# Performance work log

Measured on AMD Instinct MI355X. Metric: run time of the kernel, lower is better.

The kernel has to match this reference:

```python
import jax, jax.numpy as jnp
import numpy as np

B, T, C, NH = 4, 2048, 1024, 16
HD = C // NH  # head dim = 64


def setup_inputs() -> dict:
    key = jax.random.key(0)
    ks = jax.random.split(key, 5)
    s = 0.02
    return {
        "x": jax.random.normal(ks[0], (B, T, C), dtype=jnp.float32),
        "W_attn": jax.random.normal(ks[1], (C, 3 * C), dtype=jnp.float32) * s,
        "b_attn": jnp.zeros((3 * C,), dtype=jnp.float32),
        "W_proj": jax.random.normal(ks[2], (C, C), dtype=jnp.float32) * s,
        "b_proj": jnp.zeros((C,), dtype=jnp.float32),
    }


def reference(x, W_attn, b_attn, W_proj, b_proj):
    Bv, Tv, Cv = x.shape
    qkv = x @ W_attn + b_attn  # [B,T,3C]
    q, k, v = jnp.split(qkv, 3, axis=2)
    # [B,T,C] -> [B,NH,T,HD]
    def heads(t):
        return t.reshape(Bv, Tv, NH, HD).transpose(0, 2, 1, 3)
    q, k, v = heads(q), heads(k), heads(v)
    scores = jnp.einsum("bhqd,bhkd->bhqk", q, k) / jnp.sqrt(jnp.float32(HD))
    causal = jnp.tril(jnp.ones((Tv, Tv), dtype=bool))
    scores = jnp.where(causal[None, None, :, :], scores, jnp.float32(-jnp.inf))
    probs = jax.nn.softmax(scores, axis=-1)
    # dropout rate is 0.0 -> identity
    y = jnp.einsum("bhqk,bhkd->bhqd", probs, v)
    y = y.transpose(0, 2, 1, 3).reshape(Bv, Tv, Cv)
    return y @ W_proj + b_proj
```

## Files before the change

### kernel.cpp

```cpp
#include <hip/hip_runtime.h>
#include <hip/hip_bf16.h>

#define Bsz 4
#define Tseq 2048
#define Cdim 1024
#define NH 16
#define HD 64
#define Mrows (Bsz*Tseq)
#define N3C (3*Cdim)

typedef __attribute__((ext_vector_type(8))) short short8;
typedef __attribute__((ext_vector_type(4))) short short4v;
typedef __attribute__((ext_vector_type(4))) float float4v;

__device__ __forceinline__ unsigned short f2b(float f) {
    union { float f; unsigned u; } x; x.f = f;
    unsigned u = x.u;
    u += 0x7fff + ((u >> 16) & 1);
    return (unsigned short)(u >> 16);
}

__device__ __forceinline__ unsigned pk2bf(float a, float b) {
#if __has_builtin(__builtin_amdgcn_cvt_pk_bf16_f32)
    auto w = __builtin_amdgcn_cvt_pk_bf16_f32(a, b);
    unsigned u; __builtin_memcpy(&u, &w, 4);
    return u;
#else
    return (unsigned)f2b(a) | ((unsigned)f2b(b) << 16);
#endif
}

#define GLDS(gp, lp) __builtin_amdgcn_global_load_lds(                         \
    (const __attribute__((address_space(1))) unsigned*)(gp),                   \
    (__attribute__((address_space(3))) unsigned*)(lp), 16, 0, 0)

__global__ __launch_bounds__(256) void cast_kernel(const float* __restrict__ in,
                                                   unsigned short* __restrict__ out, int n) {
    int i = (blockIdx.x * 256 + threadIdx.x) * 4;
    if (i < n) {
        float4 v = *reinterpret_cast<const float4*>(in + i);
        ushort4 o;
        o.x = f2b(v.x); o.y = f2b(v.y); o.z = f2b(v.z); o.w = f2b(v.w);
        *reinterpret_cast<ushort4*>(out + i) = o;
    }
}

__global__ __launch_bounds__(256) void transpose_cast(const float* __restrict__ in,
                                                      unsigned short* __restrict__ out,
                                                      int K, int N) {
    __shared__ float tile[32][33];
    int n0 = blockIdx.x * 32, k0 = blockIdx.y * 32;
    int tx = threadIdx.x & 31, ty = threadIdx.x >> 5;
    #pragma unroll
    for (int i = 0; i < 32; i += 8)
        tile[ty + i][tx] = in[(k0 + ty + i) * N + n0 + tx];
    __syncthreads();
    #pragma unroll
    for (int i = 0; i < 32; i += 8)
        out[(size_t)(n0 + ty + i) * K + k0 + tx] = f2b(tile[tx][ty + i]);
}


template<bool QKV>
__global__ __launch_bounds__(512, 2) void gemm256(const unsigned short* __restrict__ A,
                                                  const unsigned short* __restrict__ Bt,
                                                  const float* __restrict__ bias,
                                                  unsigned short* __restrict__ qb,
                                                  unsigned short* __restrict__ kb,
                                                  unsigned short* __restrict__ vb,
                                                  float* __restrict__ out) {
    __shared__ unsigned short As[3][256 * 64];
    __shared__ unsigned short Bs[3][128 * 64];

    int tid = threadIdx.x;
    int lane = tid & 63, wave = tid >> 6;
    int wm = wave >> 2, wn = wave & 3;
    int l15 = lane & 15, quad = lane >> 4;
    int sx = l15 & 7;

    int f = blockIdx.x;
    int xcd = f & 7, slot = f >> 3;
    int rowblk = xcd * 4 + (slot & 3);
    int colblk = slot >> 2;
    int row0 = rowblk * 256;
    int col0 = colblk * 128;

    int srow = lane >> 3;
    int gsw = ((lane & 7) ^ srow) * 8;
    const unsigned short* Ag = A + (size_t)(row0 + wave * 32 + srow) * Cdim + gsw;
    const unsigned short* Bg = Bt + (size_t)(col0 + wave * 16 + srow) * Cdim + gsw;

    float4v acc[8][2] = {};

    #define STAGE256(kk, sb) do {                                              \
        unsigned short* Al = &As[sb][wave * 32 * 64];                          \
        unsigned short* Bl = &Bs[sb][wave * 16 * 64];                          \
        GLDS(Ag + (kk), Al);                                                   \
        GLDS(Ag + (kk) + (size_t)8  * Cdim, Al + 8 * 64);                      \
        GLDS(Ag + (kk) + (size_t)16 * Cdim, Al + 16 * 64);                     \
        GLDS(Ag + (kk) + (size_t)24 * Cdim, Al + 24 * 64);                     \
        GLDS(Bg + (kk), Bl);                                                   \
        GLDS(Bg + (kk) + (size_t)8  * Cdim, Bl + 8 * 64);                      \
    } while (0)

    STAGE256(0, 0);
    STAGE256(64, 1);
    asm volatile("s_waitcnt vmcnt(6)" ::: "memory");
    __builtin_amdgcn_s_barrier();

    int bc = 0, bp = 2;
    #pragma unroll 1
    for (int t = 0; t < 16; ++t) {
        int kpre = ((t + 2) & 15) * 64;
        STAGE256(kpre, bp);

        const unsigned short* Asb = &As[bc][0];
        const unsigned short* Bsb = &Bs[bc][0];
        #pragma unroll
        for (int kg = 0; kg < 2; kg++) {
            int gcol = ((kg * 4 + quad) ^ sx) * 8;
            short8 af[8], bf[2];
            #pragma unroll
            for (int mi = 0; mi < 8; mi++)
                af[mi] = *(const short8*)&Asb[(wm * 128 + mi * 16 + l15) * 64 + gcol];
            #pragma unroll
            for (int ni = 0; ni < 2; ni++)
                bf[ni] = *(const short8*)&Bsb[(wn * 32 + ni * 16 + l15) * 64 + gcol];
            __builtin_amdgcn_s_setprio(1);
            #pragma unroll
            for (int mi = 0; mi < 8; mi++)
                #pragma unroll
                for (int ni = 0; ni < 2; ni++)
                    acc[mi][ni] = __builtin_amdgcn_mfma_f32_16x16x32_bf16(af[mi], bf[ni], acc[mi][ni], 0, 0, 0);
            __builtin_amdgcn_s_setprio(0);
        }

        asm volatile("s_waitcnt vmcnt(6)" ::: "memory");
        __builtin_amdgcn_s_barrier();
        bc = (bc == 2) ? 0 : bc + 1;
        bp = (bp == 2) ? 0 : bp + 1;
    }
    #undef STAGE256

    #pragma unroll
    for (int mi = 0; mi < 8; mi++) {
        #pragma unroll
        for (int ni = 0; ni < 2; ni++) {
            int colb = col0 + wn * 32 + ni * 16 + l15;
            int rowb = row0 + wm * 128 + mi * 16 + quad * 4;
            if (QKV) {
                int p = colb >> 10;
                int h = (colb & 1023) >> 6;
                int d = colb & 63;
                int b = rowb >> 11;
                int t = rowb & 2047;
                if (p == 2) {
                    ushort4 pk;
                    pk.x = f2b(acc[mi][ni][0] + bias[colb]);
                    pk.y = f2b(acc[mi][ni][1] + bias[colb]);
                    pk.z = f2b(acc[mi][ni][2] + bias[colb]);
                    pk.w = f2b(acc[mi][ni][3] + bias[colb]);
                    *(ushort4*)&vb[((size_t)(b * NH + h) * HD + d) * Tseq + t] = pk;
                } else {
                    unsigned short* dst = (p == 0) ? qb : kb;
                    #pragma unroll
                    for (int r = 0; r < 4; r++)
                        dst[((size_t)(b * NH + h) * Tseq + (t + r)) * HD + d] =
                            f2b(acc[mi][ni][r] + bias[colb]);
                }
            } else {
                #pragma unroll
                for (int r = 0; r < 4; r++)
                    out[(size_t)(rowb + r) * Cdim + colb] = acc[mi][ni][r] + bias[colb];
            }
        }
    }
}


__global__ __launch_bounds__(256, 4) void attn_kernel(const unsigned short* __restrict__ qb,
                                                      const unsigned short* __restrict__ kb,
                                                      const unsigned short* __restrict__ vt,
                                                      unsigned short* __restrict__ yb) {
    __shared__ unsigned short Ks[2][64 * 64];
    __shared__ unsigned short Vs[2][64 * 64];

    int tid = threadIdx.x;
    int lane = tid & 63, wave = tid >> 6;
    int l15 = lane & 15, quad = lane >> 4;
    int bh = blockIdx.x;
    int qt = 15 - blockIdx.y;

    const unsigned short* Qh = qb + (size_t)bh * Tseq * HD;
    const unsigned short* Kh = kb + (size_t)bh * Tseq * HD;
    const unsigned short* Vh = vt + (size_t)bh * HD * Tseq;
    int b = bh >> 4, h = bh & 15;
    const float cexp = 0.18033688011112042f;

    int q0 = qt * 128;
    int rb0 = q0 + wave * 32;

    short8 qf[2][2];
    #pragma unroll
    for (int mi = 0; mi < 2; mi++)
        #pragma unroll
        for (int g = 0; g < 2; g++)
            qf[mi][g] = *(const short8*)(Qh + (size_t)(rb0 + mi * 16 + l15) * HD + g * 32 + quad * 8);

    int srow = lane >> 3;
    int scol = ((lane & 7) ^ srow) * 8;
    const unsigned short* Kg0 = Kh + (size_t)(wave * 16 + srow) * HD + scol;
    const unsigned short* Vg0 = Vh + (size_t)(wave * 16 + srow) * Tseq + scol;
    unsigned short* Kl0 = &Ks[0][wave * 1024];
    unsigned short* Vl0 = &Vs[0][wave * 1024];
    unsigned short* Kl1 = &Ks[1][wave * 1024];
    unsigned short* Vl1 = &Vs[1][wave * 1024];

    int sx = l15 & 7;
    int kx0 = (quad ^ sx) * 8;
    int kx1 = ((4 + quad) ^ sx) * 8;
    int qh_ = quad >> 1, ql_ = quad & 1;

    float4v ov[2][4] = {};
    float m[2]  = {-1e30f, -1e30f};
    float lp[2] = {0.f, 0.f};

    int nw = (q0 >> 6) + 2;

    GLDS(Kg0, Kl0);                GLDS(Kg0 + 8 * HD, Kl0 + 512);
    GLDS(Vg0, Vl0);                GLDS(Vg0 + 8 * Tseq, Vl0 + 512);
    __syncthreads();

    #pragma unroll 1
    for (int it = 0; it < nw; ++it) {
        int j0 = it << 6;

        if (it + 1 < nw) {
            int jn = j0 + 64;
            unsigned short* Kl = (it & 1) ? Kl0 : Kl1;
            unsigned short* Vl = (it & 1) ? Vl0 : Vl1;
            GLDS(Kg0 + (size_t)jn * HD, Kl);
            GLDS(Kg0 + (size_t)(jn + 8) * HD, Kl + 512);
            GLDS(Vg0 + jn, Vl);
            GLDS(Vg0 + 8 * Tseq + jn, Vl + 512);
        }

        if (j0 <= rb0 + 31) {
            const unsigned short* Kl = &Ks[it & 1][0];
            const unsigned short* Vl = &Vs[it & 1][0];

            float4v st[2][4];
            #pragma unroll
            for (int mi = 0; mi < 2; mi++)
                #pragma unroll
                for (int kg = 0; kg < 4; kg++)
                    st[mi][kg] = (float4v){0.f, 0.f, 0.f, 0.f};
            #pragma unroll
            for (int kg = 0; kg < 4; kg++) {
                int krow = kg * 1024 + l15 * 64;
                short8 kf0 = *(const short8*)&Kl[krow + kx0];
                short8 kf1 = *(const short8*)&Kl[krow + kx1];
                st[0][kg] = __builtin_amdgcn_mfma_f32_16x16x32_bf16(kf0, qf[0][0], st[0][kg], 0, 0, 0);
                st[0][kg] = __builtin_amdgcn_mfma_f32_16x16x32_bf16(kf1, qf[0][1], st[0][kg], 0, 0, 0);
                st[1][kg] = __builtin_amdgcn_mfma_f32_16x16x32_bf16(kf0, qf[1][0], st[1][kg], 0, 0, 0);
                st[1][kg] = __builtin_amdgcn_mfma_f32_16x16x32_bf16(kf1, qf[1][1], st[1][kg], 0, 0, 0);
            }

            if (j0 + 63 > rb0) {
                #pragma unroll
                for (int mi = 0; mi < 2; mi++) {
                    int qrow = rb0 + mi * 16 + l15;
                    #pragma unroll
                    for (int kg = 0; kg < 4; kg++) {
                        int keyb = j0 + kg * 16 + quad * 4;
                        #pragma unroll
                        for (int r = 0; r < 4; r++)
                            if (keyb + r > qrow) st[mi][kg][r] = -1e30f;
                    }
                }
            }

            short4v pf[2][4];
            #pragma unroll
            for (int mi = 0; mi < 2; mi++) {
                float mx = st[mi][0][0];
                #pragma unroll
                for (int kg = 0; kg < 4; kg++)
                    #pragma unroll
                    for (int r = 0; r < 4; r++)
                        mx = fmaxf(mx, st[mi][kg][r]);
                mx = fmaxf(mx, __shfl_xor(mx, 16));
                mx = fmaxf(mx, __shfl_xor(mx, 32));
                if (__any(mx > m[mi] + 16.0f)) {
                    float mn = fmaxf(m[mi], mx);
                    float alv = __builtin_amdgcn_exp2f((m[mi] - mn) * cexp);
                    m[mi] = mn;
                    lp[mi] *= alv;
                    float ar_[4];
                    #pragma unroll
                    for (int r = 0; r < 4; r++)
                        ar_[r] = __shfl(alv, quad * 4 + r);
                    #pragma unroll
                    for (int dg = 0; dg < 4; dg++)
                        #pragma unroll
                        for (int r = 0; r < 4; r++)
                            ov[mi][dg][r] *= ar_[r];
                }
                float mc = -m[mi] * cexp;
                float sum = 0.f;
                #pragma unroll
                for (int kg = 0; kg < 4; kg++) {
                    float p0 = __builtin_amdgcn_exp2f(__builtin_fmaf(st[mi][kg][0], cexp, mc));
                    float p1 = __builtin_amdgcn_exp2f(__builtin_fmaf(st[mi][kg][1], cexp, mc));
                    float p2 = __builtin_amdgcn_exp2f(__builtin_fmaf(st[mi][kg][2], cexp, mc));
                    float p3 = __builtin_amdgcn_exp2f(__builtin_fmaf(st[mi][kg][3], cexp, mc));
                    sum += (p0 + p1) + (p2 + p3);
                    union { unsigned u[2]; short4v s; } pk_;
                    pk_.u[0] = pk2bf(p0, p1);
                    pk_.u[1] = pk2bf(p2, p3);
                    pf[mi][kg] = pk_.s;
                }
                lp[mi] += sum;
            }

            #pragma unroll
            for (int kg = 0; kg < 4; kg++) {
                int vx = (((kg * 2 + qh_) ^ sx) << 3) + ql_ * 4;
                #pragma unroll
                for (int dg = 0; dg < 4; dg++) {
                    short4v vf = *(const short4v*)&Vl[dg * 1024 + l15 * 64 + vx];
                    ov[0][dg] = __builtin_amdgcn_mfma_f32_16x16x16bf16_1k(pf[0][kg], vf, ov[0][dg], 0, 0, 0);
                    ov[1][dg] = __builtin_amdgcn_mfma_f32_16x16x16bf16_1k(pf[1][kg], vf, ov[1][dg], 0, 0, 0);
                }
            }
        }

        __syncthreads();
    }

    #pragma unroll
    for (int mi = 0; mi < 2; mi++) {
        float lf = lp[mi];
        lf += __shfl_xor(lf, 16);
        lf += __shfl_xor(lf, 32);
        float rinv[4];
        #pragma unroll
        for (int r = 0; r < 4; r++)
            rinv[r] = 1.0f / __shfl(lf, quad * 4 + r);
        #pragma unroll
        for (int dg = 0; dg < 4; dg++)
            #pragma unroll
            for (int r = 0; r < 4; r++) {
                int t = rb0 + mi * 16 + quad * 4 + r;
                yb[((size_t)b * Tseq + t) * Cdim + h * HD + dg * 16 + l15] =
                    f2b(ov[mi][dg][r] * rinv[r]);
            }
    }
}

extern "C" void kernel_launch(void* const* d_in, const int* in_sizes, int n_in,
                              void* d_out, int out_size, void* d_ws, size_t ws_size,
                              hipStream_t stream) {
    const float* x  = (const float*)d_in[0];
    const float* Wa = (const float*)d_in[1];
    const float* ba = (const float*)d_in[2];
    const float* Wp = (const float*)d_in[3];
    const float* bp = (const float*)d_in[4];
    float* out = (float*)d_out;

    unsigned short* ws = (unsigned short*)d_ws;
    unsigned short* xb  = ws;
    unsigned short* Wat = xb  + (size_t)Mrows * Cdim;
    unsigned short* Wpt = Wat + (size_t)N3C * Cdim;
    unsigned short* qb  = Wpt + (size_t)Cdim * Cdim;
    unsigned short* kb  = qb  + (size_t)Bsz * NH * Tseq * HD;
    unsigned short* vb  = kb  + (size_t)Bsz * NH * Tseq * HD;
    unsigned short* yb  = vb  + (size_t)Bsz * NH * Tseq * HD;

    int nx = Mrows * Cdim;
    cast_kernel<<<nx / 4 / 256, 256, 0, stream>>>(x, xb, nx);
    transpose_cast<<<dim3(N3C / 32, Cdim / 32), 256, 0, stream>>>(Wa, Wat, Cdim, N3C);
    transpose_cast<<<dim3(Cdim / 32, Cdim / 32), 256, 0, stream>>>(Wp, Wpt, Cdim, Cdim);

    gemm256<true><<<768, 512, 0, stream>>>(xb, Wat, ba, qb, kb, vb, nullptr);

    attn_kernel<<<dim3(Bsz * NH, 16), 256, 0, stream>>>(qb, kb, vb, yb);

    gemm256<false><<<256, 512, 0, stream>>>(yb, Wpt, bp, nullptr, nullptr, nullptr, out);
}
```

Before: 265.9 us.

## Add 256x256-tile QKV GEMM with eight-phase ping-pong LDS pipeline

```diff
diff --git a/kernel.cpp b/kernel.cpp
--- a/kernel.cpp
+++ b/kernel.cpp
@@ -62,6 +62,184 @@
 
 
 template<bool QKV>
+__global__ __launch_bounds__(512, 2) void gemm8p(const unsigned short* __restrict__ A,
+                                                 const unsigned short* __restrict__ Bt,
+                                                 const float* __restrict__ bias,
+                                                 unsigned short* __restrict__ qb,
+                                                 unsigned short* __restrict__ kb,
+                                                 unsigned short* __restrict__ vb,
+                                                 float* __restrict__ out) {
+    __shared__ unsigned short As[2][256 * 64];
+    __shared__ unsigned short Bs[2][256 * 64];
+
+    int tid = threadIdx.x;
+    int lane = tid & 63, wave = tid >> 6;
+    int wm = wave >> 2, wn = wave & 3;
+    int l15 = lane & 15, quad = lane >> 4;
+    int sx = l15 & 7;
+
+    int f = blockIdx.x;
+    int xcd = f & 7, slot = f >> 3;
+    int rowblk = xcd * 4 + (slot & 3);
+    int colblk = slot >> 2;
+    int row0 = rowblk * 256;
+    int col0 = colblk * 256;
+
+    int srow = lane >> 3;
+    int gsw = ((lane & 7) ^ srow) * 8;
+    const unsigned short* Ag = A + (size_t)(row0 + srow) * Cdim + gsw;
+    const unsigned short* Bg = Bt + (size_t)(col0 + srow) * Cdim + gsw;
+
+    #define STG_A(h, kk, nb) do {                                               \
+        unsigned short* L = &As[nb][((h) * 128 + wave * 8) * 64];               \
+        GLDS(Ag + (size_t)((h) * 128 + wave * 8) * Cdim + (kk), L);             \
+        GLDS(Ag + (size_t)((h) * 128 + 64 + wave * 8) * Cdim + (kk), L + 64 * 64); \
+    } while (0)
+    #define STG_B(h, kk, nb) do {                                               \
+        unsigned short* L = &Bs[nb][((h) * 128 + wave * 8) * 64];               \
+        GLDS(Bg + (size_t)((h) * 128 + wave * 8) * Cdim + (kk), L);             \
+        GLDS(Bg + (size_t)((h) * 128 + 64 + wave * 8) * Cdim + (kk), L + 64 * 64); \
+    } while (0)
+
+    float4v acc[8][4] = {};
+    short8 af0[8], af1[8];
+
+    STG_A(0, 0, 0); STG_A(1, 0, 0); STG_B(0, 0, 0); STG_B(1, 0, 0);
+    asm volatile("s_waitcnt vmcnt(0)" ::: "memory");
+    __builtin_amdgcn_s_barrier();
+
+    int gc0 = (quad ^ sx) * 8;
+    int gc1 = ((4 + quad) ^ sx) * 8;
+
+    #pragma unroll 1
+    for (int t = 0; t < 16; ++t) {
+        int b = t & 1, nb = b ^ 1;
+        int kn = ((t + 1) & 15) * 64;
+        const unsigned short* Asb = &As[b][0];
+        const unsigned short* Bsb = &Bs[b][0];
+
+        {
+            short8 bf[2];
+            #pragma unroll
+            for (int mi = 0; mi < 8; mi++)
+                af0[mi] = *(const short8*)&Asb[(wm * 128 + mi * 16 + l15) * 64 + gc0];
+            #pragma unroll
+            for (int ni = 0; ni < 2; ni++)
+                bf[ni] = *(const short8*)&Bsb[(wn * 64 + ni * 16 + l15) * 64 + gc0];
+            STG_A(0, kn, nb);
+            __builtin_amdgcn_s_barrier();
+            asm volatile("s_waitcnt lgkmcnt(0)" ::: "memory");
+            __builtin_amdgcn_sched_barrier(0);
+            __builtin_amdgcn_s_setprio(1);
+            #pragma unroll
+            for (int mi = 0; mi < 8; mi++)
+                #pragma unroll
+                for (int ni = 0; ni < 2; ni++)
+                    acc[mi][ni] = __builtin_amdgcn_mfma_f32_16x16x32_bf16(af0[mi], bf[ni], acc[mi][ni], 0, 0, 0);
+            __builtin_amdgcn_s_setprio(0);
+            __builtin_amdgcn_s_barrier();
+        }
+        {
+            short8 bf[2];
+            #pragma unroll
+            for (int mi = 0; mi < 8; mi++)
+                af1[mi] = *(const short8*)&Asb[(wm * 128 + mi * 16 + l15) * 64 + gc1];
+            #pragma unroll
+            for (int ni = 0; ni < 2; ni++)
+                bf[ni] = *(const short8*)&Bsb[(wn * 64 + ni * 16 + l15) * 64 + gc1];
+            STG_A(1, kn, nb);
+            asm volatile("s_waitcnt vmcnt(4)" ::: "memory");
+            __builtin_amdgcn_s_barrier();
+            asm volatile("s_waitcnt lgkmcnt(0)" ::: "memory");
+            __builtin_amdgcn_sched_barrier(0);
+            __builtin_amdgcn_s_setprio(1);
+            #pragma unroll
+            for (int mi = 0; mi < 8; mi++)
+                #pragma unroll
+                for (int ni = 0; ni < 2; ni++)
+                    acc[mi][ni] = __builtin_amdgcn_mfma_f32_16x16x32_bf16(af1[mi], bf[ni], acc[mi][ni], 0, 0, 0);
+            __builtin_amdgcn_s_setprio(0);
+            __builtin_amdgcn_s_barrier();
+        }
+        {
+            short8 bf[2];
+            #pragma unroll
+            for (int ni = 0; ni < 2; ni++)
+                bf[ni] = *(const short8*)&Bsb[(wn * 64 + 32 + ni * 16 + l15) * 64 + gc1];
+            STG_B(0, kn, nb);
+            __builtin_amdgcn_s_barrier();
+            asm volatile("s_waitcnt lgkmcnt(0)" ::: "memory");
+            __builtin_amdgcn_sched_barrier(0);
+            __builtin_amdgcn_s_setprio(1);
+            #pragma unroll
+            for (int mi = 0; mi < 8; mi++)
+                #pragma unroll
+                for (int ni = 0; ni < 2; ni++)
+                    acc[mi][2 + ni] = __builtin_amdgcn_mfma_f32_16x16x32_bf16(af1[mi], bf[ni], acc[mi][2 + ni], 0, 0, 0);
+            __builtin_amdgcn_s_setprio(0);
+            __builtin_amdgcn_s_barrier();
+        }
+        {
+            short8 bf[2];
+            #pragma unroll
+            for (int ni = 0; ni < 2; ni++)
+                bf[ni] = *(const short8*)&Bsb[(wn * 64 + 32 + ni * 16 + l15) * 64 + gc0];
+            STG_B(1, kn, nb);
+            asm volatile("s_waitcnt vmcnt(2)" ::: "memory");
+            __builtin_amdgcn_s_barrier();
+            asm volatile("s_waitcnt lgkmcnt(0)" ::: "memory");
+            __builtin_amdgcn_sched_barrier(0);
+            __builtin_amdgcn_s_setprio(1);
+            #pragma unroll
+            for (int mi = 0; mi < 8; mi++)
+                #pragma unroll
+                for (int ni = 0; ni < 2; ni++)
+                    acc[mi][2 + ni] = __builtin_amdgcn_mfma_f32_16x16x32_bf16(af0[mi], bf[ni], acc[mi][2 + ni], 0, 0, 0);
+            __builtin_amdgcn_s_setprio(0);
+            __builtin_amdgcn_s_barrier();
+        }
+    }
+    asm volatile("s_waitcnt vmcnt(0)" ::: "memory");
+    #undef STG_A
+    #undef STG_B
+
+    #pragma unroll
+    for (int mi = 0; mi < 8; mi++) {
+        #pragma unroll
+        for (int nj = 0; nj < 4; nj++) {
+            int colb = col0 + wn * 64 + nj * 16 + l15;
+            int rowb = row0 + wm * 128 + mi * 16 + quad * 4;
+            if (QKV) {
+                int p = colb >> 10;
+                int h = (colb & 1023) >> 6;
+                int d = colb & 63;
+                int b = rowb >> 11;
+                int t = rowb & 2047;
+                if (p == 2) {
+                    ushort4 pk;
+                    pk.x = f2b(acc[mi][nj][0] + bias[colb]);
+                    pk.y = f2b(acc[mi][nj][1] + bias[colb]);
+                    pk.z = f2b(acc[mi][nj][2] + bias[colb]);
+                    pk.w = f2b(acc[mi][nj][3] + bias[colb]);
+                    *(ushort4*)&vb[((size_t)(b * NH + h) * HD + d) * Tseq + t] = pk;
+                } else {
+                    unsigned short* dst = (p == 0) ? qb : kb;
+                    #pragma unroll
+                    for (int r = 0; r < 4; r++)
+                        dst[((size_t)(b * NH + h) * Tseq + (t + r)) * HD + d] =
+                            f2b(acc[mi][nj][r] + bias[colb]);
+                }
+            } else {
+                #pragma unroll
+                for (int r = 0; r < 4; r++)
+                    out[(size_t)(rowb + r) * Cdim + colb] = acc[mi][nj][r] + bias[colb];
+            }
+        }
+    }
+}
+
+
+template<bool QKV>
 __global__ __launch_bounds__(512, 2) void gemm256(const unsigned short* __restrict__ A,
                                                   const unsigned short* __restrict__ Bt,
                                                   const float* __restrict__ bias,
@@ -140,6 +318,7 @@
         bc = (bc == 2) ? 0 : bc + 1;
         bp = (bp == 2) ? 0 : bp + 1;
     }
+    asm volatile("s_waitcnt vmcnt(0)" ::: "memory");
     #undef STAGE256
 
     #pragma unroll
@@ -382,7 +561,7 @@
     transpose_cast<<<dim3(N3C / 32, Cdim / 32), 256, 0, stream>>>(Wa, Wat, Cdim, N3C);
     transpose_cast<<<dim3(Cdim / 32, Cdim / 32), 256, 0, stream>>>(Wp, Wpt, Cdim, Cdim);
 
-    gemm256<true><<<768, 512, 0, stream>>>(xb, Wat, ba, qb, kb, vb, nullptr);
+    gemm8p<true><<<384, 512, 0, stream>>>(xb, Wat, ba, qb, kb, vb, nullptr);
 
     attn_kernel<<<dim3(Bsz * NH, 16), 256, 0, stream>>>(qb, kb, vb, yb);
 
```

New measurement: 256.5 us. 1.04x faster.

## Restructure GEMM into four-phase ping-pong schedule with square 64x64 wave tiles

Applied to the files above, without the earlier changes.

```diff
diff --git a/kernel.cpp b/kernel.cpp
--- a/kernel.cpp
+++ b/kernel.cpp
@@ -62,19 +62,19 @@
 
 
 template<bool QKV>
-__global__ __launch_bounds__(512, 2) void gemm256(const unsigned short* __restrict__ A,
-                                                  const unsigned short* __restrict__ Bt,
-                                                  const float* __restrict__ bias,
-                                                  unsigned short* __restrict__ qb,
-                                                  unsigned short* __restrict__ kb,
-                                                  unsigned short* __restrict__ vb,
-                                                  float* __restrict__ out) {
+__global__ __launch_bounds__(512, 2) void gemm4p(const unsigned short* __restrict__ A,
+                                                 const unsigned short* __restrict__ Bt,
+                                                 const float* __restrict__ bias,
+                                                 unsigned short* __restrict__ qb,
+                                                 unsigned short* __restrict__ kb,
+                                                 unsigned short* __restrict__ vb,
+                                                 float* __restrict__ out) {
     __shared__ unsigned short As[3][256 * 64];
     __shared__ unsigned short Bs[3][128 * 64];
 
     int tid = threadIdx.x;
     int lane = tid & 63, wave = tid >> 6;
-    int wm = wave >> 2, wn = wave & 3;
+    int wm = wave >> 1, wn = wave & 1;
     int l15 = lane & 15, quad = lane >> 4;
     int sx = l15 & 7;
 
@@ -87,67 +87,134 @@
 
     int srow = lane >> 3;
     int gsw = ((lane & 7) ^ srow) * 8;
-    const unsigned short* Ag = A + (size_t)(row0 + wave * 32 + srow) * Cdim + gsw;
-    const unsigned short* Bg = Bt + (size_t)(col0 + wave * 16 + srow) * Cdim + gsw;
-
-    float4v acc[8][2] = {};
-
-    #define STAGE256(kk, sb) do {                                              \
-        unsigned short* Al = &As[sb][wave * 32 * 64];                          \
-        unsigned short* Bl = &Bs[sb][wave * 16 * 64];                          \
-        GLDS(Ag + (kk), Al);                                                   \
-        GLDS(Ag + (kk) + (size_t)8  * Cdim, Al + 8 * 64);                      \
-        GLDS(Ag + (kk) + (size_t)16 * Cdim, Al + 16 * 64);                     \
-        GLDS(Ag + (kk) + (size_t)24 * Cdim, Al + 24 * 64);                     \
-        GLDS(Bg + (kk), Bl);                                                   \
-        GLDS(Bg + (kk) + (size_t)8  * Cdim, Bl + 8 * 64);                      \
+    const unsigned short* Ag = A + (size_t)(row0 + srow) * Cdim + gsw;
+    const unsigned short* Bg = Bt + (size_t)(col0 + srow) * Cdim + gsw;
+
+    #define STG_A(c, kk, sb)                                                    \
+        GLDS(Ag + (size_t)((c) * 64 + wave * 8) * Cdim + (kk),                  \
+             &As[sb][((c) * 64 + wave * 8) * 64])
+    #define STG_B(c, kk, sb)                                                    \
+        GLDS(Bg + (size_t)((c) * 64 + wave * 8) * Cdim + (kk),                  \
+             &Bs[sb][((c) * 64 + wave * 8) * 64])
+    #define STG_ALL(kk, sb) do {                                                \
+        STG_A(0, kk, sb); STG_A(1, kk, sb); STG_A(2, kk, sb); STG_A(3, kk, sb); \
+        STG_B(0, kk, sb); STG_B(1, kk, sb);                                     \
     } while (0)
 
-    STAGE256(0, 0);
-    STAGE256(64, 1);
+    float4v acc[4][4] = {};
+    short8 af0[4], af1[4];
+
+    STG_ALL(0, 0);
+    STG_ALL(64, 1);
     asm volatile("s_waitcnt vmcnt(6)" ::: "memory");
     __builtin_amdgcn_s_barrier();
+
+    int gc0 = (quad ^ sx) * 8;
+    int gc1 = ((4 + quad) ^ sx) * 8;
+    int arow = (wm * 64 + l15) * 64;
+    int brow = (wn * 64 + l15) * 64;
 
     int bc = 0, bp = 2;
     #pragma unroll 1
     for (int t = 0; t < 16; ++t) {
-        int kpre = ((t + 2) & 15) * 64;
-        STAGE256(kpre, bp);
-
+        int kn = ((t + 2) & 15) * 64;
         const unsigned short* Asb = &As[bc][0];
         const unsigned short* Bsb = &Bs[bc][0];
-        #pragma unroll
-        for (int kg = 0; kg < 2; kg++) {
-            int gcol = ((kg * 4 + quad) ^ sx) * 8;
-            short8 af[8], bf[2];
-            #pragma unroll
-            for (int mi = 0; mi < 8; mi++)
-                af[mi] = *(const short8*)&Asb[(wm * 128 + mi * 16 + l15) * 64 + gcol];
-            #pragma unroll
-            for (int ni = 0; ni < 2; ni++)
-                bf[ni] = *(const short8*)&Bsb[(wn * 32 + ni * 16 + l15) * 64 + gcol];
+
+        {
+            short8 bf[2];
+            #pragma unroll
+            for (int mi = 0; mi < 4; mi++)
+                af0[mi] = *(const short8*)&Asb[arow + mi * 1024 + gc0];
+            #pragma unroll
+            for (int nj = 0; nj < 2; nj++)
+                bf[nj] = *(const short8*)&Bsb[brow + nj * 1024 + gc0];
+            STG_A(0, kn, bp); STG_A(1, kn, bp);
+            __builtin_amdgcn_s_barrier();
+            asm volatile("s_waitcnt lgkmcnt(0)" ::: "memory");
+            __builtin_amdgcn_sched_barrier(0);
             __builtin_amdgcn_s_setprio(1);
             #pragma unroll
-            for (int mi = 0; mi < 8; mi++)
-                #pragma unroll
-                for (int ni = 0; ni < 2; ni++)
-                    acc[mi][ni] = __builtin_amdgcn_mfma_f32_16x16x32_bf16(af[mi], bf[ni], acc[mi][ni], 0, 0, 0);
+            for (int mi = 0; mi < 4; mi++)
+                #pragma unroll
+                for (int nj = 0; nj < 2; nj++)
+                    acc[mi][nj] = __builtin_amdgcn_mfma_f32_16x16x32_bf16(af0[mi], bf[nj], acc[mi][nj], 0, 0, 0);
             __builtin_amdgcn_s_setprio(0);
-        }
-
-        asm volatile("s_waitcnt vmcnt(6)" ::: "memory");
-        __builtin_amdgcn_s_barrier();
+            __builtin_amdgcn_s_barrier();
+        }
+        {
+            short8 bf[2];
+            #pragma unroll
+            for (int mi = 0; mi < 4; mi++)
+                af1[mi] = *(const short8*)&Asb[arow + mi * 1024 + gc1];
+            #pragma unroll
+            for (int nj = 0; nj < 2; nj++)
+                bf[nj] = *(const short8*)&Bsb[brow + nj * 1024 + gc1];
+            STG_A(2, kn, bp); STG_A(3, kn, bp);
+            __builtin_amdgcn_s_barrier();
+            asm volatile("s_waitcnt lgkmcnt(0)" ::: "memory");
+            __builtin_amdgcn_sched_barrier(0);
+            __builtin_amdgcn_s_setprio(1);
+            #pragma unroll
+            for (int mi = 0; mi < 4; mi++)
+                #pragma unroll
+                for (int nj = 0; nj < 2; nj++)
+                    acc[mi][nj] = __builtin_amdgcn_mfma_f32_16x16x32_bf16(af1[mi], bf[nj], acc[mi][nj], 0, 0, 0);
+            __builtin_amdgcn_s_setprio(0);
+            __builtin_amdgcn_s_barrier();
+        }
+        {
+            short8 bf[2];
+            #pragma unroll
+            for (int nj = 0; nj < 2; nj++)
+                bf[nj] = *(const short8*)&Bsb[brow + (2 + nj) * 1024 + gc1];
+            STG_B(0, kn, bp);
+            __builtin_amdgcn_s_barrier();
+            asm volatile("s_waitcnt lgkmcnt(0)" ::: "memory");
+            __builtin_amdgcn_sched_barrier(0);
+            __builtin_amdgcn_s_setprio(1);
+            #pragma unroll
+            for (int mi = 0; mi < 4; mi++)
+                #pragma unroll
+                for (int nj = 0; nj < 2; nj++)
+                    acc[mi][2 + nj] = __builtin_amdgcn_mfma_f32_16x16x32_bf16(af1[mi], bf[nj], acc[mi][2 + nj], 0, 0, 0);
+            __builtin_amdgcn_s_setprio(0);
+            __builtin_amdgcn_s_barrier();
+        }
+        {
+            short8 bf[2];
+            #pragma unroll
+            for (int nj = 0; nj < 2; nj++)
+                bf[nj] = *(const short8*)&Bsb[brow + (2 + nj) * 1024 + gc0];
+            STG_B(1, kn, bp);
+            __builtin_amdgcn_s_barrier();
+            asm volatile("s_waitcnt lgkmcnt(0)" ::: "memory");
+            __builtin_amdgcn_sched_barrier(0);
+            __builtin_amdgcn_s_setprio(1);
+            #pragma unroll
+            for (int mi = 0; mi < 4; mi++)
+                #pragma unroll
+                for (int nj = 0; nj < 2; nj++)
+                    acc[mi][2 + nj] = __builtin_amdgcn_mfma_f32_16x16x32_bf16(af0[mi], bf[nj], acc[mi][2 + nj], 0, 0, 0);
+            __builtin_amdgcn_s_setprio(0);
+            asm volatile("s_waitcnt vmcnt(6)" ::: "memory");
+            __builtin_amdgcn_s_barrier();
+        }
+
         bc = (bc == 2) ? 0 : bc + 1;
         bp = (bp == 2) ? 0 : bp + 1;
     }
-    #undef STAGE256
+    asm volatile("s_waitcnt vmcnt(0)" ::: "memory");
+    #undef STG_A
+    #undef STG_B
+    #undef STG_ALL
 
     #pragma unroll
-    for (int mi = 0; mi < 8; mi++) {
+    for (int mi = 0; mi < 4; mi++) {
         #pragma unroll
-        for (int ni = 0; ni < 2; ni++) {
-            int colb = col0 + wn * 32 + ni * 16 + l15;
-            int rowb = row0 + wm * 128 + mi * 16 + quad * 4;
+        for (int nj = 0; nj < 4; nj++) {
+            int colb = col0 + wn * 64 + nj * 16 + l15;
+            int rowb = row0 + wm * 64 + mi * 16 + quad * 4;
             if (QKV) {
                 int p = colb >> 10;
                 int h = (colb & 1023) >> 6;
@@ -156,22 +223,22 @@
                 int t = rowb & 2047;
                 if (p == 2) {
                     ushort4 pk;
-                    pk.x = f2b(acc[mi][ni][0] + bias[colb]);
-                    pk.y = f2b(acc[mi][ni][1] + bias[colb]);
-                    pk.z = f2b(acc[mi][ni][2] + bias[colb]);
-                    pk.w = f2b(acc[mi][ni][3] + bias[colb]);
+                    pk.x = f2b(acc[mi][nj][0] + bias[colb]);
+                    pk.y = f2b(acc[mi][nj][1] + bias[colb]);
+                    pk.z = f2b(acc[mi][nj][2] + bias[colb]);
+                    pk.w = f2b(acc[mi][nj][3] + bias[colb]);
                     *(ushort4*)&vb[((size_t)(b * NH + h) * HD + d) * Tseq + t] = pk;
                 } else {
                     unsigned short* dst = (p == 0) ? qb : kb;
                     #pragma unroll
                     for (int r = 0; r < 4; r++)
                         dst[((size_t)(b * NH + h) * Tseq + (t + r)) * HD + d] =
-                            f2b(acc[mi][ni][r] + bias[colb]);
+                            f2b(acc[mi][nj][r] + bias[colb]);
                 }
             } else {
                 #pragma unroll
                 for (int r = 0; r < 4; r++)
-                    out[(size_t)(rowb + r) * Cdim + colb] = acc[mi][ni][r] + bias[colb];
+                    out[(size_t)(rowb + r) * Cdim + colb] = acc[mi][nj][r] + bias[colb];
             }
         }
     }
@@ -382,9 +449,9 @@
     transpose_cast<<<dim3(N3C / 32, Cdim / 32), 256, 0, stream>>>(Wa, Wat, Cdim, N3C);
     transpose_cast<<<dim3(Cdim / 32, Cdim / 32), 256, 0, stream>>>(Wp, Wpt, Cdim, Cdim);
 
-    gemm256<true><<<768, 512, 0, stream>>>(xb, Wat, ba, qb, kb, vb, nullptr);
+    gemm4p<true><<<768, 512, 0, stream>>>(xb, Wat, ba, qb, kb, vb, nullptr);
 
     attn_kernel<<<dim3(Bsz * NH, 16), 256, 0, stream>>>(qb, kb, vb, yb);
 
-    gemm256<false><<<256, 512, 0, stream>>>(yb, Wpt, bp, nullptr, nullptr, nullptr, out);
-}
+    gemm4p<false><<<256, 512, 0, stream>>>(yb, Wpt, bp, nullptr, nullptr, nullptr, out);
+}
```

New measurement: 262.0 us. About the same (-1.5%).

## Restructure GEMMs into templated two-phase pipeline with larger tiles

Applied to the files above, without the earlier changes.

```diff
diff --git a/kernel.cpp b/kernel.cpp
--- a/kernel.cpp
+++ b/kernel.cpp
@@ -61,93 +61,109 @@
 }
 
 
-template<bool QKV>
-__global__ __launch_bounds__(512, 2) void gemm256(const unsigned short* __restrict__ A,
-                                                  const unsigned short* __restrict__ Bt,
-                                                  const float* __restrict__ bias,
-                                                  unsigned short* __restrict__ qb,
-                                                  unsigned short* __restrict__ kb,
-                                                  unsigned short* __restrict__ vb,
-                                                  float* __restrict__ out) {
-    __shared__ unsigned short As[3][256 * 64];
-    __shared__ unsigned short Bs[3][128 * 64];
+template<int MI, int BN, bool QKV>
+__global__ __launch_bounds__(512, 2) void gemm2p(const unsigned short* __restrict__ A,
+                                                 const unsigned short* __restrict__ Bt,
+                                                 const float* __restrict__ bias,
+                                                 unsigned short* __restrict__ qb,
+                                                 unsigned short* __restrict__ kb,
+                                                 unsigned short* __restrict__ vb,
+                                                 float* __restrict__ out) {
+    __shared__ unsigned short As[2][2][256 * 32];
+    __shared__ unsigned short Bs[2][2][BN * 32];
+
+    constexpr int WN = (MI == 8) ? 4 : 2;
+    constexpr int SPP = 2 + BN / 128;
+    constexpr int NCOLB = (QKV ? N3C : Cdim) / BN;
 
     int tid = threadIdx.x;
     int lane = tid & 63, wave = tid >> 6;
-    int wm = wave >> 2, wn = wave & 3;
+    int wm = wave / WN, wn = wave % WN;
     int l15 = lane & 15, quad = lane >> 4;
-    int sx = l15 & 7;
+    int wmBase = wm * (MI * 16);
 
     int f = blockIdx.x;
     int xcd = f & 7, slot = f >> 3;
     int rowblk = xcd * 4 + (slot & 3);
     int colblk = slot >> 2;
     int row0 = rowblk * 256;
-    int col0 = colblk * 128;
-
-    int srow = lane >> 3;
-    int gsw = ((lane & 7) ^ srow) * 8;
-    const unsigned short* Ag = A + (size_t)(row0 + wave * 32 + srow) * Cdim + gsw;
-    const unsigned short* Bg = Bt + (size_t)(col0 + wave * 16 + srow) * Cdim + gsw;
-
-    float4v acc[8][2] = {};
-
-    #define STAGE256(kk, sb) do {                                              \
-        unsigned short* Al = &As[sb][wave * 32 * 64];                          \
-        unsigned short* Bl = &Bs[sb][wave * 16 * 64];                          \
-        GLDS(Ag + (kk), Al);                                                   \
-        GLDS(Ag + (kk) + (size_t)8  * Cdim, Al + 8 * 64);                      \
-        GLDS(Ag + (kk) + (size_t)16 * Cdim, Al + 16 * 64);                     \
-        GLDS(Ag + (kk) + (size_t)24 * Cdim, Al + 24 * 64);                     \
-        GLDS(Bg + (kk), Bl);                                                   \
-        GLDS(Bg + (kk) + (size_t)8  * Cdim, Bl + 8 * 64);                      \
+    int col0 = colblk * BN;
+    (void)NCOLB;
+
+    int srow4 = lane >> 2;
+    int gsrc = ((lane & 3) ^ ((lane >> 3) & 3)) * 8;
+    const unsigned short* Ag = A + (size_t)(row0 + srow4) * Cdim + gsrc;
+    const unsigned short* Bg = Bt + (size_t)(col0 + srow4) * Cdim + gsrc;
+
+    #define STG_AB(sph_, kk_, sb_) do {                                         \
+        GLDS(Ag + (size_t)(wave * 16) * Cdim + (kk_),                           \
+             &As[sb_][sph_][(wave * 16) * 32]);                                 \
+        GLDS(Ag + (size_t)(128 + wave * 16) * Cdim + (kk_),                     \
+             &As[sb_][sph_][(128 + wave * 16) * 32]);                           \
+        GLDS(Bg + (size_t)(wave * 16) * Cdim + (kk_),                           \
+             &Bs[sb_][sph_][(wave * 16) * 32]);                                 \
+        if constexpr (BN == 256)                                                \
+            GLDS(Bg + (size_t)(128 + wave * 16) * Cdim + (kk_),                 \
+                 &Bs[sb_][sph_][(128 + wave * 16) * 32]);                       \
     } while (0)
 
-    STAGE256(0, 0);
-    STAGE256(64, 1);
-    asm volatile("s_waitcnt vmcnt(6)" ::: "memory");
+    float4v acc[MI][4] = {};
+
+    STG_AB(0, 0, 0);
+    STG_AB(1, 32, 0);
+    STG_AB(0, 64, 1);
+    if constexpr (SPP == 4) asm volatile("s_waitcnt vmcnt(8)" ::: "memory");
+    else                    asm volatile("s_waitcnt vmcnt(6)" ::: "memory");
     __builtin_amdgcn_s_barrier();
 
-    int bc = 0, bp = 2;
+    int gq0 = (quad ^ ((l15 >> 1) & 3)) * 8;
+    int afb = (wmBase + l15) * 32 + gq0;
+    int bfb = (wn * 64 + l15) * 32 + gq0;
+
     #pragma unroll 1
     for (int t = 0; t < 16; ++t) {
-        int kpre = ((t + 2) & 15) * 64;
-        STAGE256(kpre, bp);
-
-        const unsigned short* Asb = &As[bc][0];
-        const unsigned short* Bsb = &Bs[bc][0];
         #pragma unroll
-        for (int kg = 0; kg < 2; kg++) {
-            int gcol = ((kg * 4 + quad) ^ sx) * 8;
-            short8 af[8], bf[2];
-            #pragma unroll
-            for (int mi = 0; mi < 8; mi++)
-                af[mi] = *(const short8*)&Asb[(wm * 128 + mi * 16 + l15) * 64 + gcol];
-            #pragma unroll
-            for (int ni = 0; ni < 2; ni++)
-                bf[ni] = *(const short8*)&Bsb[(wn * 32 + ni * 16 + l15) * 64 + gcol];
+        for (int ph = 0; ph < 2; ++ph) {
+            int bc = t & 1;
+            const unsigned short* Asl = &As[bc][ph][0];
+            const unsigned short* Bsl = &Bs[bc][ph][0];
+
+            short8 af[MI], bf[4];
+            #pragma unroll
+            for (int mi = 0; mi < MI; mi++)
+                af[mi] = *(const short8*)&Asl[afb + mi * 512];
+            #pragma unroll
+            for (int nj = 0; nj < 4; nj++)
+                bf[nj] = *(const short8*)&Bsl[bfb + nj * 512];
+
+            int s = (2 * t + ph + 3) & 31;
+            int st_ = s >> 1, sph = s & 1, sb = st_ & 1;
+            STG_AB(sph, st_ * 64 + sph * 32, sb);
+
+            if constexpr (SPP == 4) asm volatile("s_waitcnt vmcnt(8)" ::: "memory");
+            else                    asm volatile("s_waitcnt vmcnt(6)" ::: "memory");
+            __builtin_amdgcn_s_barrier();
+            asm volatile("s_waitcnt lgkmcnt(0)" ::: "memory");
+            __builtin_amdgcn_sched_barrier(0);
             __builtin_amdgcn_s_setprio(1);
             #pragma unroll
-            for (int mi = 0; mi < 8; mi++)
-                #pragma unroll
-                for (int ni = 0; ni < 2; ni++)
-                    acc[mi][ni] = __builtin_amdgcn_mfma_f32_16x16x32_bf16(af[mi], bf[ni], acc[mi][ni], 0, 0, 0);
+            for (int mi = 0; mi < MI; mi++)
+                #pragma unroll
+                for (int nj = 0; nj < 4; nj++)
+                    acc[mi][nj] = __builtin_amdgcn_mfma_f32_16x16x32_bf16(af[mi], bf[nj], acc[mi][nj], 0, 0, 0);
             __builtin_amdgcn_s_setprio(0);
+            __builtin_amdgcn_s_barrier();
         }
-
-        asm volatile("s_waitcnt vmcnt(6)" ::: "memory");
-        __builtin_amdgcn_s_barrier();
-        bc = (bc == 2) ? 0 : bc + 1;
-        bp = (bp == 2) ? 0 : bp + 1;
     }
-    #undef STAGE256
+    asm volatile("s_waitcnt vmcnt(0)" ::: "memory");
+    #undef STG_AB
 
     #pragma unroll
-    for (int mi = 0; mi < 8; mi++) {
+    for (int mi = 0; mi < MI; mi++) {
         #pragma unroll
-        for (int ni = 0; ni < 2; ni++) {
-            int colb = col0 + wn * 32 + ni * 16 + l15;
-            int rowb = row0 + wm * 128 + mi * 16 + quad * 4;
+        for (int nj = 0; nj < 4; nj++) {
+            int colb = col0 + wn * 64 + nj * 16 + l15;
+            int rowb = row0 + wmBase + mi * 16 + quad * 4;
             if (QKV) {
                 int p = colb >> 10;
                 int h = (colb & 1023) >> 6;
@@ -156,22 +172,22 @@
                 int t = rowb & 2047;
                 if (p == 2) {
                     ushort4 pk;
-                    pk.x = f2b(acc[mi][ni][0] + bias[colb]);
-                    pk.y = f2b(acc[mi][ni][1] + bias[colb]);
-                    pk.z = f2b(acc[mi][ni][2] + bias[colb]);
-                    pk.w = f2b(acc[mi][ni][3] + bias[colb]);
+                    pk.x = f2b(acc[mi][nj][0] + bias[colb]);
+                    pk.y = f2b(acc[mi][nj][1] + bias[colb]);
+                    pk.z = f2b(acc[mi][nj][2] + bias[colb]);
+                    pk.w = f2b(acc[mi][nj][3] + bias[colb]);
                     *(ushort4*)&vb[((size_t)(b * NH + h) * HD + d) * Tseq + t] = pk;
                 } else {
                     unsigned short* dst = (p == 0) ? qb : kb;
                     #pragma unroll
                     for (int r = 0; r < 4; r++)
                         dst[((size_t)(b * NH + h) * Tseq + (t + r)) * HD + d] =
-                            f2b(acc[mi][ni][r] + bias[colb]);
+                            f2b(acc[mi][nj][r] + bias[colb]);
                 }
             } else {
                 #pragma unroll
                 for (int r = 0; r < 4; r++)
-                    out[(size_t)(rowb + r) * Cdim + colb] = acc[mi][ni][r] + bias[colb];
+                    out[(size_t)(rowb + r) * Cdim + colb] = acc[mi][nj][r] + bias[colb];
             }
         }
     }
@@ -382,9 +398,9 @@
     transpose_cast<<<dim3(N3C / 32, Cdim / 32), 256, 0, stream>>>(Wa, Wat, Cdim, N3C);
     transpose_cast<<<dim3(Cdim / 32, Cdim / 32), 256, 0, stream>>>(Wp, Wpt, Cdim, Cdim);
 
-    gemm256<true><<<768, 512, 0, stream>>>(xb, Wat, ba, qb, kb, vb, nullptr);
+    gemm2p<8, 256, true><<<384, 512, 0, stream>>>(xb, Wat, ba, qb, kb, vb, nullptr);
 
     attn_kernel<<<dim3(Bsz * NH, 16), 256, 0, stream>>>(qb, kb, vb, yb);
 
-    gemm256<false><<<256, 512, 0, stream>>>(yb, Wpt, bp, nullptr, nullptr, nullptr, out);
-}
+    gemm2p<4, 128, false><<<256, 512, 0, stream>>>(yb, Wpt, bp, nullptr, nullptr, nullptr, out);
+}
```

Result: faster. 253.9 us (-4.5%).
